# Optimization experiments

Hardware: AMD Instinct MI355X
Metric: run time of the kernel (lower is better)

The kernel has to match this reference:

```python
import jax, jax.numpy as jnp
import numpy as np

B, E, T, H = 2, 1024, 2048, 16
DH = E // H


def _conv1x1(x, W, b, mask):
    # x: [B,C,T], W: [O,C], b: [O], mask: [B,1,T] (norm=False -> plain conv on masked input)
    x = x * mask
    return jnp.einsum('oc,bct->bot', W, x) + b[None, :, None]


def setup_inputs() -> dict:
    key = jax.random.key(0)
    ks = jax.random.split(key, 16)
    inp = {
        'q': jax.random.normal(ks[0], (B, E, T), jnp.float32),
        'k': jax.random.normal(ks[1], (B, E, T), jnp.float32),
        'v': jax.random.normal(ks[2], (B, E, T), jnp.float32),
        'query_mask': (jax.random.uniform(ks[3], (B, 1, T)) < 0.9).astype(jnp.float32),
        'key_mask': (jax.random.uniform(ks[4], (B, 1, T)) < 0.9).astype(jnp.float32),
        'value_mask': (jax.random.uniform(ks[5], (B, 1, T)) < 0.9).astype(jnp.float32),
        'Wq': jax.random.normal(ks[6], (E, E), jnp.float32) * (1.0 / np.sqrt(E)),
        'bq': jnp.zeros((E,), jnp.float32),
        'Wk': jax.random.normal(ks[7], (E, E), jnp.float32) * (1.0 / np.sqrt(E)),
        'bk': jnp.zeros((E,), jnp.float32),
        'Wv': jax.random.normal(ks[8], (E, E), jnp.float32) * (1.0 / np.sqrt(E)),
        'bv': jnp.zeros((E,), jnp.float32),
        'Wo': jax.random.normal(ks[9], (E, E), jnp.float32) * (1.0 / np.sqrt(E)),
        'bo': jnp.zeros((E,), jnp.float32),
    }
    return inp


def reference(q, k, v, query_mask, key_mask, value_mask, Wq, bq, Wk, bk, Wv, bv, Wo, bo):
    # 1x1 conv projections with input masking (norm=False path)
    qp = _conv1x1(q, Wq, bq, query_mask)   # [B,E,T]
    kp = _conv1x1(k, Wk, bk, key_mask)
    vp = _conv1x1(v, Wv, bv, value_mask)
    # split heads: [B,E,T] -> [B,H,DH,T]
    qh = qp.reshape(B, H, DH, T)
    kh = kp.reshape(B, H, DH, T)
    vh = vp.reshape(B, H, DH, T)
    # scores = q^T k with pre-softmax multiplicative masks, scaled by sqrt(embed_dim)
    scores = jnp.einsum('bhdq,bhdk->bhqk', qh, kh)
    scores = scores * query_mask[:, :, :, None] * key_mask[:, :, None, :] / np.sqrt(E)
    attn = jax.nn.softmax(scores, axis=-1) * key_mask[:, :, None, :]  # post-softmax mask
    # transpose_scores=False path: v @ scores (contracts v's time dim with the query dim)
    out = jnp.einsum('bhdq,bhqk->bhdk', vh, attn)  # [B,H,DH,T]
    out = out.reshape(B, E, T)
    return _conv1x1(out, Wo, bo, key_mask)
```

## Files before the change

kernel.cpp:

```cpp
#include <hip/hip_runtime.h>

#define B 2
#define E 1024
#define T 2048
#define H 16
#define DH 64

#define SCALE2 0.0450842200277801f

typedef _Float16 f16x8 __attribute__((ext_vector_type(8)));
typedef float f32x4 __attribute__((ext_vector_type(4)));
typedef float f32x16 __attribute__((ext_vector_type(16)));
typedef unsigned short ushort8v __attribute__((ext_vector_type(8)));
typedef unsigned int uint4v __attribute__((ext_vector_type(4)));

__device__ __forceinline__ f32x4 mfma16(f16x8 a, f16x8 b, f32x4 c) {
  return __builtin_amdgcn_mfma_f32_16x16x32_f16(a, b, c, 0, 0, 0);
}
__device__ __forceinline__ f32x16 mfma32(f16x8 a, f16x8 b, f32x16 c) {
  return __builtin_amdgcn_mfma_f32_32x32x16_f16(a, b, c, 0, 0, 0);
}
__device__ __forceinline__ unsigned short f16u(float x) {
  _Float16 h = (_Float16)x;
  return __builtin_bit_cast(unsigned short, h);
}
__device__ __forceinline__ float ex2(float x) {
  return __builtin_amdgcn_exp2f(x);
}
__device__ __forceinline__ unsigned int pk16(float a, float b) {
  auto h = __builtin_amdgcn_cvt_pkrtz(a, b);
  return __builtin_bit_cast(unsigned int, h);
}

__global__ __launch_bounds__(256) void prep_weights(
    const float* __restrict__ Wq, const float* __restrict__ Wk,
    const float* __restrict__ Wv, const float* __restrict__ Wo,
    unsigned short* __restrict__ WqB, unsigned short* __restrict__ WkB,
    unsigned short* __restrict__ WvB, unsigned short* __restrict__ WoB) {
  const int which = blockIdx.y;
  const int i = (blockIdx.x * 256 + threadIdx.x) * 4;
  const float* src = which == 0 ? Wq : which == 1 ? Wk : which == 2 ? Wv : Wo;
  unsigned short* dst = which == 0 ? WqB : which == 1 ? WkB : which == 2 ? WvB : WoB;
  float4 v = *(const float4*)&src[i];
  ((unsigned int*)&dst[i])[0] = f16u(v.x) | ((unsigned)f16u(v.y) << 16);
  ((unsigned int*)&dst[i])[1] = f16u(v.z) | ((unsigned)f16u(v.w) << 16);
}

__global__ __launch_bounds__(256) void transpose_cvt(
    const float* __restrict__ q, const float* __restrict__ k,
    const float* __restrict__ v, unsigned short* __restrict__ XtQ,
    unsigned short* __restrict__ XtK, unsigned short* __restrict__ XtV) {
  __shared__ float Xs[32 * 36];
  const int z = blockIdx.z, which = z >> 1, b = z & 1;
  const float* X = which == 0 ? q : which == 1 ? k : v;
  unsigned short* O = which == 0 ? XtQ : which == 1 ? XtK : XtV;
  const int e0 = blockIdx.y * 32, t0 = blockIdx.x * 32;
  const int tid = threadIdx.x;
  const int r = tid >> 3, c = (tid & 7) * 4;
  *(float4*)&Xs[r * 36 + c] = *(const float4*)&X[((size_t)b * E + e0 + r) * T + t0 + c];
  __syncthreads();
  unsigned short h[4];
#pragma unroll
  for (int j = 0; j < 4; ++j) h[j] = f16u(Xs[(c + j) * 36 + r]);
  const size_t o = ((size_t)b * T + t0 + r) * E + e0 + c;
  ((unsigned int*)&O[o])[0] = h[0] | ((unsigned)h[1] << 16);
  ((unsigned int*)&O[o])[1] = h[2] | ((unsigned)h[3] << 16);
}

__global__ __launch_bounds__(256) void proj_qkv(
    const unsigned short* __restrict__ WqB, const unsigned short* __restrict__ WkB,
    const unsigned short* __restrict__ WvB, const unsigned short* __restrict__ XtQ,
    const unsigned short* __restrict__ XtK, const unsigned short* __restrict__ XtV,
    const float* __restrict__ bq, const float* __restrict__ bk,
    const float* __restrict__ bv, const float* __restrict__ qmask,
    const float* __restrict__ kmask, const float* __restrict__ vmask,
    unsigned short* __restrict__ qp2, unsigned short* __restrict__ kp2,
    unsigned short* __restrict__ vp) {
  __shared__ unsigned short Ah[128 * 72], Bs[128 * 72];
  const int b = blockIdx.z, my = blockIdx.y;
  const int which = my >> 3, o0 = (my & 7) * 128, t0 = blockIdx.x * 128;
  const unsigned short* W = which == 0 ? WqB : which == 1 ? WkB : WvB;
  const unsigned short* Xt = which == 0 ? XtQ : which == 1 ? XtK : XtV;
  const float* bias = which == 0 ? bq : which == 1 ? bk : bv;
  const float* mask = which == 0 ? qmask : which == 1 ? kmask : vmask;

  const int tid = threadIdx.x, wave = tid >> 6, lane = tid & 63;
  const int lg = lane & 15, quad = lane >> 4;
  const int wm = (wave & 1) * 64, wn = (wave >> 1) * 64;
  const int sr = tid >> 3, sc = (tid & 7) * 8;

  f32x4 acc[4][4];
#pragma unroll
  for (int i = 0; i < 4; ++i)
#pragma unroll
    for (int j = 0; j < 4; ++j) acc[i][j] = (f32x4){0.f, 0.f, 0.f, 0.f};

  for (int k0 = 0; k0 < E; k0 += 64) {
    ushort8v ra[4], rb[4];
#pragma unroll
    for (int p = 0; p < 4; ++p) {
      ra[p] = *(const ushort8v*)&W[(size_t)(o0 + p * 32 + sr) * E + k0 + sc];
      rb[p] = *(const ushort8v*)&Xt[((size_t)b * T + t0 + p * 32 + sr) * E + k0 + sc];
    }
    __syncthreads();
#pragma unroll
    for (int p = 0; p < 4; ++p) {
      *(ushort8v*)&Ah[(p * 32 + sr) * 72 + sc] = ra[p];
      *(ushort8v*)&Bs[(p * 32 + sr) * 72 + sc] = rb[p];
    }
    __syncthreads();
    f16x8 af[4][2];
#pragma unroll
    for (int mt = 0; mt < 4; ++mt) {
      af[mt][0] = *(const f16x8*)&Ah[(wm + mt * 16 + lg) * 72 + quad * 8];
      af[mt][1] = *(const f16x8*)&Ah[(wm + mt * 16 + lg) * 72 + 32 + quad * 8];
    }
#pragma unroll
    for (int nt = 0; nt < 4; ++nt) {
      f16x8 b0 = *(const f16x8*)&Bs[(wn + nt * 16 + lg) * 72 + quad * 8];
      f16x8 b1 = *(const f16x8*)&Bs[(wn + nt * 16 + lg) * 72 + 32 + quad * 8];
#pragma unroll
      for (int mt = 0; mt < 4; ++mt) {
        f32x4 c = acc[mt][nt];
        c = mfma16(af[mt][0], b0, c);
        c = mfma16(af[mt][1], b1, c);
        acc[mt][nt] = c;
      }
    }
  }
#pragma unroll
  for (int nt = 0; nt < 4; ++nt) {
    const int tcol = t0 + wn + nt * 16 + lg;
    const float mv = mask[b * T + tcol];
#pragma unroll
    for (int mt = 0; mt < 4; ++mt) {
      const int oF = o0 + wm + mt * 16 + quad * 4;
      float v4[4];
      if (which == 0) {
        const float s = mv * SCALE2;
#pragma unroll
        for (int r = 0; r < 4; ++r) v4[r] = (acc[mt][nt][r] + bias[oF + r]) * s;
      } else if (which == 1) {
#pragma unroll
        for (int r = 0; r < 4; ++r) v4[r] = (acc[mt][nt][r] + bias[oF + r]) * mv;
      } else {
#pragma unroll
        for (int r = 0; r < 4; ++r) v4[r] = acc[mt][nt][r] * mv + bias[oF + r];
      }
      if (which <= 1) {
        unsigned short* O = which == 0 ? qp2 : kp2;
        const int head = (o0 + wm) >> 6;
        const int bh2 = b * H + head;
        const size_t idx8 =
            (((size_t)(bh2 * (T / 32) + (tcol >> 5)) * 4 + mt) * 32 + (tcol & 31)) * 2 +
            (quad >> 1);
        unsigned int* dst = (unsigned int*)(O + idx8 * 8 + (quad & 1) * 4);
        dst[0] = f16u(v4[0]) | ((unsigned)f16u(v4[1]) << 16);
        dst[1] = f16u(v4[2]) | ((unsigned)f16u(v4[3]) << 16);
      } else {
#pragma unroll
        for (int r = 0; r < 4; ++r)
          vp[((size_t)b * E + oF + r) * T + tcol] = f16u(v4[r]);
      }
    }
  }
}

__global__ __launch_bounds__(256) void repack_v(
    const unsigned short* __restrict__ vp, unsigned short* __restrict__ vp2) {
  __shared__ unsigned short Ls[64 * 136];
  const int q0 = blockIdx.x * 128, hh = blockIdx.y, b = blockIdx.z;
  const int bh = b * H + hh;
  const int tid = threadIdx.x;
#pragma unroll
  for (int w = 0; w < 2; ++w) {
    const int d = w * 32 + (tid >> 3);
    const int c = (tid & 7) * 16;
    const unsigned short* src = vp + ((size_t)b * E + hh * DH + d) * T + q0 + c;
    *(ushort8v*)&Ls[d * 136 + c] = *(const ushort8v*)src;
    *(ushort8v*)&Ls[d * 136 + c + 8] = *(const ushort8v*)(src + 8);
  }
  __syncthreads();
#pragma unroll
  for (int w = 0; w < 4; ++w) {
    const int flat = w * 256 + tid;
    const int hb = flat & 1, lnv = (flat >> 1) & 31, dt = (flat >> 6) & 1,
              qgl = flat >> 7;
    ushort8v val = *(const ushort8v*)&Ls[(dt * 32 + lnv) * 136 + qgl * 16 + hb * 8];
    const size_t idx8 =
        (((size_t)(bh * (T / 16) + (q0 >> 4) + qgl) * 2 + dt) * 32 + lnv) * 2 + hb;
    *(ushort8v*)&vp2[idx8 * 8] = val;
  }
}

__global__ __launch_bounds__(256) void attn_stats(
    const unsigned short* __restrict__ qp2, const unsigned short* __restrict__ kp2,
    float* __restrict__ lLogOut) {
  const int bh = blockIdx.y;
  const int q0 = blockIdx.x * 128;
  const int tid = threadIdx.x, wave = tid >> 6, lane = tid & 63;
  const int ln = lane & 31, half = lane >> 5;

  const int t32q = (q0 >> 5) + wave;
  f16x8 aq[4];
#pragma unroll
  for (int s = 0; s < 4; ++s)
    aq[s] = *(const f16x8*)&qp2[((((size_t)bh * (T / 32) + t32q) * 4 + s) * 64 +
                                 ln * 2 + half) * 8];

  float lacc[16];
#pragma unroll
  for (int r = 0; r < 16; ++r) lacc[r] = 0.f;

  f16x8 bkr[2][4];
#pragma unroll
  for (int nt = 0; nt < 2; ++nt)
#pragma unroll
    for (int s = 0; s < 4; ++s)
      bkr[nt][s] = *(const f16x8*)&kp2[((((size_t)bh * (T / 32) + nt) * 4 + s) * 64 +
                                        ln * 2 + half) * 8];

  for (int kt = 0; kt < T; kt += 64) {
    const int kn = (kt + 64) & (T - 1);
    f16x8 nb[2][4];
#pragma unroll
    for (int nt = 0; nt < 2; ++nt)
#pragma unroll
      for (int s = 0; s < 4; ++s)
        nb[nt][s] =
            *(const f16x8*)&kp2[((((size_t)bh * (T / 32) + (kn >> 5) + nt) * 4 + s) * 64 +
                                 ln * 2 + half) * 8];
    f32x16 S0 = {}, S1 = {};
#pragma unroll
    for (int s = 0; s < 4; ++s) {
      S0 = mfma32(aq[s], bkr[0][s], S0);
      S1 = mfma32(aq[s], bkr[1][s], S1);
    }
#pragma unroll
    for (int r = 0; r < 16; ++r) lacc[r] += ex2(S0[r]) + ex2(S1[r]);
#pragma unroll
    for (int nt = 0; nt < 2; ++nt)
#pragma unroll
      for (int s = 0; s < 4; ++s) bkr[nt][s] = nb[nt][s];
  }
#pragma unroll
  for (int off = 1; off < 32; off <<= 1)
#pragma unroll
    for (int r = 0; r < 16; ++r) lacc[r] += __shfl_xor(lacc[r], off, 64);
  if (ln == 0) {
#pragma unroll
    for (int t = 0; t < 4; ++t) {
      f32x4 o;
#pragma unroll
      for (int j = 0; j < 4; ++j) o[j] = -__builtin_amdgcn_logf(lacc[t * 4 + j]);
      *(f32x4*)&lLogOut[(size_t)bh * T + q0 + wave * 32 + t * 8 + half * 4] = o;
    }
  }
}

__global__ __launch_bounds__(256) void attn_apply(
    const unsigned short* __restrict__ qp2, const unsigned short* __restrict__ kp2,
    const unsigned short* __restrict__ vp2, const float* __restrict__ lLog,
    unsigned short* __restrict__ ao) {
  __shared__ float st[32 * 130];
  const int bh = blockIdx.y, b = bh >> 4, h = bh & 15;
  const int kblk = blockIdx.x * 64;
  const int tid = threadIdx.x, wave = tid >> 6, lane = tid & 63;
  const int ln = lane & 31, half = lane >> 5;
  const int kt = wave & 1, qh = wave >> 1;

  const int t32k = (kblk >> 5) + kt;
  f16x8 bkk[4];
#pragma unroll
  for (int s = 0; s < 4; ++s)
    bkk[s] = *(const f16x8*)&kp2[((((size_t)bh * (T / 32) + t32k) * 4 + s) * 64 +
                                  ln * 2 + half) * 8];

  f32x16 acc0 = {}, acc1 = {};
  const int qstart = qh * (T / 2);

  f16x8 aqN[4], avN[2][2];
#pragma unroll
  for (int s = 0; s < 4; ++s)
    aqN[s] = *(const f16x8*)&qp2[((((size_t)bh * (T / 32) + (qstart >> 5)) * 4 + s) * 64 +
                                  ln * 2 + half) * 8];
#pragma unroll
  for (int dt = 0; dt < 2; ++dt)
#pragma unroll
    for (int f = 0; f < 2; ++f)
      avN[dt][f] = *(const f16x8*)&vp2[((((size_t)bh * (T / 16) + (qstart >> 4) + f) * 2 +
                                         dt) * 32 + ln) * 16 + half * 8];

  for (int qt = qstart; qt < qstart + T / 2; qt += 32) {
    f16x8 aq[4], av[2][2];
#pragma unroll
    for (int s = 0; s < 4; ++s) aq[s] = aqN[s];
#pragma unroll
    for (int dt = 0; dt < 2; ++dt)
#pragma unroll
      for (int f = 0; f < 2; ++f) av[dt][f] = avN[dt][f];
    const int qn = qt + 32 < qstart + T / 2 ? qt + 32 : qstart;
#pragma unroll
    for (int s = 0; s < 4; ++s)
      aqN[s] = *(const f16x8*)&qp2[((((size_t)bh * (T / 32) + (qn >> 5)) * 4 + s) * 64 +
                                    ln * 2 + half) * 8];
#pragma unroll
    for (int dt = 0; dt < 2; ++dt)
#pragma unroll
      for (int f = 0; f < 2; ++f)
        avN[dt][f] = *(const f16x8*)&vp2[((((size_t)bh * (T / 16) + (qn >> 4) + f) * 2 +
                                           dt) * 32 + ln) * 16 + half * 8];
    f32x4 ll[4];
#pragma unroll
    for (int t = 0; t < 4; ++t)
      ll[t] = *(const f32x4*)&lLog[(size_t)bh * T + qt + t * 8 + half * 4];
    f32x16 S = {};
#pragma unroll
    for (int s = 0; s < 4; ++s) S = mfma32(aq[s], bkk[s], S);
    unsigned int w[8];
#pragma unroll
    for (int p = 0; p < 8; ++p) {
      const float e0 = ex2(S[p * 2 + 0] + ll[p >> 1][(p & 1) * 2 + 0]);
      const float e1 = ex2(S[p * 2 + 1] + ll[p >> 1][(p & 1) * 2 + 1]);
      w[p] = pk16(e0, e1);
    }
    unsigned int x[8];
#pragma unroll
    for (int p = 0; p < 8; ++p) x[p] = __shfl_xor(w[p], 32, 64);
    uint4v f0, f1;
    f0[0] = half ? x[2] : w[0];
    f0[1] = half ? x[3] : w[1];
    f0[2] = half ? w[2] : x[0];
    f0[3] = half ? w[3] : x[1];
    f1[0] = half ? x[6] : w[4];
    f1[1] = half ? x[7] : w[5];
    f1[2] = half ? w[6] : x[4];
    f1[3] = half ? w[7] : x[5];
    const f16x8 pf0 = __builtin_bit_cast(f16x8, f0);
    const f16x8 pf1 = __builtin_bit_cast(f16x8, f1);
    acc0 = mfma32(av[0][0], pf0, acc0);
    acc0 = mfma32(av[0][1], pf1, acc0);
    acc1 = mfma32(av[1][0], pf0, acc1);
    acc1 = mfma32(av[1][1], pf1, acc1);
  }

  __syncthreads();
  if (qh == 1) {
#pragma unroll
    for (int i = 0; i < 16; ++i) {
      st[i * 130 + kt * 65 + lane] = acc0[i];
      st[(16 + i) * 130 + kt * 65 + lane] = acc1[i];
    }
  }
  __syncthreads();
  if (qh == 0) {
#pragma unroll
    for (int i = 0; i < 16; ++i) {
      acc0[i] += st[i * 130 + kt * 65 + lane];
      acc1[i] += st[(16 + i) * 130 + kt * 65 + lane];
    }
    const int kcol = kblk + kt * 32 + ln;
    const size_t obase = ((size_t)b * T + kcol) * E + h * DH;
#pragma unroll
    for (int dt = 0; dt < 2; ++dt) {
      const float* a = dt ? (const float*)&acc1 : (const float*)&acc0;
#pragma unroll
      for (int t = 0; t < 4; ++t) {
        uint2 wv;
        wv.x = f16u(a[t * 4 + 0]) | ((unsigned)f16u(a[t * 4 + 1]) << 16);
        wv.y = f16u(a[t * 4 + 2]) | ((unsigned)f16u(a[t * 4 + 3]) << 16);
        *(uint2*)&ao[obase + dt * 32 + t * 8 + half * 4] = wv;
      }
    }
  }
}

__global__ __launch_bounds__(256) void proj_final(
    const unsigned short* __restrict__ WoB, const unsigned short* __restrict__ ao,
    const float* __restrict__ bo, const float* __restrict__ kmask,
    float* __restrict__ out) {
  __shared__ unsigned short As[64 * 68], Bs[128 * 68];
  const int b = blockIdx.z, o0 = blockIdx.y * 64, t0 = blockIdx.x * 128;
  const int tid = threadIdx.x, wave = tid >> 6, lane = tid & 63;
  const int ln = lane & 31, half = lane >> 5;
  const int wn = wave * 32;
  const int ar = tid >> 2, ac = (tid & 3) * 16;
  const int br = tid >> 1, bc = (tid & 1) * 32;

  f32x16 acc0 = {}, acc1 = {};

  for (int k0 = 0; k0 < E; k0 += 64) {
    ushort8v a0 = *(const ushort8v*)&WoB[(size_t)(o0 + ar) * E + k0 + ac];
    ushort8v a1 = *(const ushort8v*)&WoB[(size_t)(o0 + ar) * E + k0 + ac + 8];
    ushort8v b0 = *(const ushort8v*)&ao[((size_t)b * T + t0 + br) * E + k0 + bc];
    ushort8v b1 = *(const ushort8v*)&ao[((size_t)b * T + t0 + br) * E + k0 + bc + 8];
    ushort8v b2 = *(const ushort8v*)&ao[((size_t)b * T + t0 + br) * E + k0 + bc + 16];
    ushort8v b3 = *(const ushort8v*)&ao[((size_t)b * T + t0 + br) * E + k0 + bc + 24];
    __syncthreads();
    *(ushort8v*)&As[ar * 68 + ac] = a0;
    *(ushort8v*)&As[ar * 68 + ac + 8] = a1;
    *(ushort8v*)&Bs[br * 68 + bc] = b0;
    *(ushort8v*)&Bs[br * 68 + bc + 8] = b1;
    *(ushort8v*)&Bs[br * 68 + bc + 16] = b2;
    *(ushort8v*)&Bs[br * 68 + bc + 24] = b3;
    __syncthreads();
#pragma unroll
    for (int s = 0; s < 4; ++s) {
      f16x8 af0 = *(const f16x8*)&As[ln * 68 + s * 16 + half * 8];
      f16x8 af1 = *(const f16x8*)&As[(32 + ln) * 68 + s * 16 + half * 8];
      f16x8 bf = *(const f16x8*)&Bs[(wn + ln) * 68 + s * 16 + half * 8];
      acc0 = mfma32(af0, bf, acc0);
      acc1 = mfma32(af1, bf, acc1);
    }
  }
  const int tcol = t0 + wn + ln;
  const float mv = kmask[b * T + tcol];
#pragma unroll
  for (int dt = 0; dt < 2; ++dt) {
    const float* a = dt ? (const float*)&acc1 : (const float*)&acc0;
#pragma unroll
    for (int t = 0; t < 4; ++t)
#pragma unroll
      for (int j = 0; j < 4; ++j) {
        const int e = o0 + dt * 32 + t * 8 + half * 4 + j;
        out[((size_t)b * E + e) * T + tcol] = a[t * 4 + j] * mv + bo[e];
      }
  }
}

extern "C" void kernel_launch(void* const* d_in, const int* in_sizes, int n_in,
                              void* d_out, int out_size, void* d_ws, size_t ws_size,
                              hipStream_t stream) {
  const float* q = (const float*)d_in[0];
  const float* k = (const float*)d_in[1];
  const float* v = (const float*)d_in[2];
  const float* qmask = (const float*)d_in[3];
  const float* kmask = (const float*)d_in[4];
  const float* vmask = (const float*)d_in[5];
  const float* Wq = (const float*)d_in[6];
  const float* bq = (const float*)d_in[7];
  const float* Wk = (const float*)d_in[8];
  const float* bk = (const float*)d_in[9];
  const float* Wv = (const float*)d_in[10];
  const float* bv = (const float*)d_in[11];
  const float* Wo = (const float*)d_in[12];
  const float* bo = (const float*)d_in[13];

  char* w = (char*)d_ws;
  const size_t WB = (size_t)E * E * sizeof(unsigned short);
  const size_t TB = (size_t)B * T * E * sizeof(unsigned short);
  unsigned short* WqB = (unsigned short*)(w + 0 * WB);
  unsigned short* WkB = (unsigned short*)(w + 1 * WB);
  unsigned short* WvB = (unsigned short*)(w + 2 * WB);
  unsigned short* WoB = (unsigned short*)(w + 3 * WB);
  size_t off = 4 * WB;
  unsigned short* XtQ = (unsigned short*)(w + off); off += TB;
  unsigned short* XtK = (unsigned short*)(w + off); off += TB;
  unsigned short* XtV = (unsigned short*)(w + off); off += TB;
  unsigned short* qp2 = (unsigned short*)(w + off); off += TB;
  unsigned short* kp2 = (unsigned short*)(w + off); off += TB;
  unsigned short* vp  = (unsigned short*)(w + off); off += TB;
  unsigned short* vp2 = (unsigned short*)(w + off); off += TB;
  float* lLog = (float*)(w + off); off += (size_t)B * H * T * sizeof(float);
  unsigned short* ao = XtQ;

  dim3 bl(256);
  prep_weights<<<dim3((E * E) / 1024, 4), bl, 0, stream>>>(
      Wq, Wk, Wv, Wo, WqB, WkB, WvB, WoB);
  transpose_cvt<<<dim3(T / 32, E / 32, 3 * B), bl, 0, stream>>>(
      q, k, v, XtQ, XtK, XtV);
  proj_qkv<<<dim3(T / 128, 24, B), bl, 0, stream>>>(
      WqB, WkB, WvB, XtQ, XtK, XtV, bq, bk, bv, qmask, kmask, vmask, qp2, kp2, vp);
  repack_v<<<dim3(T / 128, H, B), bl, 0, stream>>>(vp, vp2);
  attn_stats<<<dim3(T / 128, B * H), bl, 0, stream>>>(qp2, kp2, lLog);
  attn_apply<<<dim3(T / 64, B * H), bl, 0, stream>>>(qp2, kp2, vp2, lLog, ao);
  proj_final<<<dim3(T / 128, E / 64, B), bl, 0, stream>>>(
      WoB, ao, bo, kmask, (float*)d_out);
}
```

Measured before the change: 284.3 us.

## Split attention stats and apply kernels across two reduction halves with merge kernels

Both attention kernels gain a z grid dimension that splits the reduction range (key range for stats, query range for apply) in two. Partial results go to fp32 scratch and are combined by two new merge kernels. This doubles the grid (512 to 1024 blocks for stats, 1024 to 2048 for apply) to fill more CUs and shortens each block's serial loop. It also swaps the shfl_xor half-exchange for permlane32_swap, prefetches the lLog row one iteration ahead, and sets a min-blocks launch bound. The cost is two extra launches and extra fp32 partial traffic, with the workspace reshuffled so aPart reuses the XtK/XtV space.

```diff
diff --git a/kernel.cpp b/kernel.cpp
--- a/kernel.cpp
+++ b/kernel.cpp
@@ -30,6 +30,11 @@
 __device__ __forceinline__ unsigned int pk16(float a, float b) {
   auto h = __builtin_amdgcn_cvt_pkrtz(a, b);
   return __builtin_bit_cast(unsigned int, h);
+}
+__device__ __forceinline__ void plswap(unsigned int& a, unsigned int& b) {
+  auto r = __builtin_amdgcn_permlane32_swap(a, b, false, false);
+  a = r[0];
+  b = r[1];
 }
 
 __global__ __launch_bounds__(256) void prep_weights(
@@ -195,8 +200,9 @@
 
 __global__ __launch_bounds__(256) void attn_stats(
     const unsigned short* __restrict__ qp2, const unsigned short* __restrict__ kp2,
-    float* __restrict__ lLogOut) {
+    float* __restrict__ sPart) {
   const int bh = blockIdx.y;
+  const int z = blockIdx.z;
   const int q0 = blockIdx.x * 128;
   const int tid = threadIdx.x, wave = tid >> 6, lane = tid & 63;
   const int ln = lane & 31, half = lane >> 5;
@@ -212,16 +218,19 @@
 #pragma unroll
   for (int r = 0; r < 16; ++r) lacc[r] = 0.f;
 
+  const int kbase = z * (T / 2);
+  const int kend = kbase + T / 2;
+
   f16x8 bkr[2][4];
 #pragma unroll
   for (int nt = 0; nt < 2; ++nt)
 #pragma unroll
     for (int s = 0; s < 4; ++s)
-      bkr[nt][s] = *(const f16x8*)&kp2[((((size_t)bh * (T / 32) + nt) * 4 + s) * 64 +
-                                        ln * 2 + half) * 8];
-
-  for (int kt = 0; kt < T; kt += 64) {
-    const int kn = (kt + 64) & (T - 1);
+      bkr[nt][s] = *(const f16x8*)&kp2[((((size_t)bh * (T / 32) + (kbase >> 5) + nt) * 4 +
+                                         s) * 64 + ln * 2 + half) * 8];
+
+  for (int kt = kbase; kt < kend; kt += 64) {
+    const int kn = (kt + 64 < kend) ? kt + 64 : kbase;
     f16x8 nb[2][4];
 #pragma unroll
     for (int nt = 0; nt < 2; ++nt)
@@ -252,18 +261,32 @@
     for (int t = 0; t < 4; ++t) {
       f32x4 o;
 #pragma unroll
-      for (int j = 0; j < 4; ++j) o[j] = -__builtin_amdgcn_logf(lacc[t * 4 + j]);
-      *(f32x4*)&lLogOut[(size_t)bh * T + q0 + wave * 32 + t * 8 + half * 4] = o;
-    }
-  }
-}
-
-__global__ __launch_bounds__(256) void attn_apply(
+      for (int j = 0; j < 4; ++j) o[j] = lacc[t * 4 + j];
+      *(f32x4*)&sPart[((size_t)z * (B * H) + bh) * T + q0 + wave * 32 + t * 8 +
+                      half * 4] = o;
+    }
+  }
+}
+
+__global__ __launch_bounds__(256) void stats_merge(
+    const float* __restrict__ sPart, float* __restrict__ lLog) {
+  const int i = (blockIdx.x * 256 + threadIdx.x) * 4;
+  const int N = B * H * T;
+  f32x4 a = *(const f32x4*)&sPart[i];
+  f32x4 b = *(const f32x4*)&sPart[N + i];
+  f32x4 o;
+#pragma unroll
+  for (int j = 0; j < 4; ++j) o[j] = -__builtin_amdgcn_logf(a[j] + b[j]);
+  *(f32x4*)&lLog[i] = o;
+}
+
+__global__ __launch_bounds__(256, 5) void attn_apply(
     const unsigned short* __restrict__ qp2, const unsigned short* __restrict__ kp2,
     const unsigned short* __restrict__ vp2, const float* __restrict__ lLog,
-    unsigned short* __restrict__ ao) {
+    float* __restrict__ aPart) {
   __shared__ float st[32 * 130];
-  const int bh = blockIdx.y, b = bh >> 4, h = bh & 15;
+  const int bh = blockIdx.y;
+  const int z = blockIdx.z;
   const int kblk = blockIdx.x * 64;
   const int tid = threadIdx.x, wave = tid >> 6, lane = tid & 63;
   const int ln = lane & 31, half = lane >> 5;
@@ -277,9 +300,11 @@
                                   ln * 2 + half) * 8];
 
   f32x16 acc0 = {}, acc1 = {};
-  const int qstart = qh * (T / 2);
+  const int qstart = (z * 2 + qh) * (T / 4);
+  const int qend = qstart + T / 4;
 
   f16x8 aqN[4], avN[2][2];
+  f32x4 llN[4];
 #pragma unroll
   for (int s = 0; s < 4; ++s)
     aqN[s] = *(const f16x8*)&qp2[((((size_t)bh * (T / 32) + (qstart >> 5)) * 4 + s) * 64 +
@@ -290,16 +315,22 @@
     for (int f = 0; f < 2; ++f)
       avN[dt][f] = *(const f16x8*)&vp2[((((size_t)bh * (T / 16) + (qstart >> 4) + f) * 2 +
                                          dt) * 32 + ln) * 16 + half * 8];
-
-  for (int qt = qstart; qt < qstart + T / 2; qt += 32) {
+#pragma unroll
+  for (int t = 0; t < 4; ++t)
+    llN[t] = *(const f32x4*)&lLog[(size_t)bh * T + qstart + t * 8 + half * 4];
+
+  for (int qt = qstart; qt < qend; qt += 32) {
     f16x8 aq[4], av[2][2];
+    f32x4 ll[4];
 #pragma unroll
     for (int s = 0; s < 4; ++s) aq[s] = aqN[s];
 #pragma unroll
     for (int dt = 0; dt < 2; ++dt)
 #pragma unroll
       for (int f = 0; f < 2; ++f) av[dt][f] = avN[dt][f];
-    const int qn = qt + 32 < qstart + T / 2 ? qt + 32 : qstart;
+#pragma unroll
+    for (int t = 0; t < 4; ++t) ll[t] = llN[t];
+    const int qn = qt + 32 < qend ? qt + 32 : qstart;
 #pragma unroll
     for (int s = 0; s < 4; ++s)
       aqN[s] = *(const f16x8*)&qp2[((((size_t)bh * (T / 32) + (qn >> 5)) * 4 + s) * 64 +
@@ -310,10 +341,9 @@
       for (int f = 0; f < 2; ++f)
         avN[dt][f] = *(const f16x8*)&vp2[((((size_t)bh * (T / 16) + (qn >> 4) + f) * 2 +
                                            dt) * 32 + ln) * 16 + half * 8];
-    f32x4 ll[4];
 #pragma unroll
     for (int t = 0; t < 4; ++t)
-      ll[t] = *(const f32x4*)&lLog[(size_t)bh * T + qt + t * 8 + half * 4];
+      llN[t] = *(const f32x4*)&lLog[(size_t)bh * T + qn + t * 8 + half * 4];
     f32x16 S = {};
 #pragma unroll
     for (int s = 0; s < 4; ++s) S = mfma32(aq[s], bkk[s], S);
@@ -324,18 +354,13 @@
       const float e1 = ex2(S[p * 2 + 1] + ll[p >> 1][(p & 1) * 2 + 1]);
       w[p] = pk16(e0, e1);
     }
-    unsigned int x[8];
-#pragma unroll
-    for (int p = 0; p < 8; ++p) x[p] = __shfl_xor(w[p], 32, 64);
+    plswap(w[0], w[2]);
+    plswap(w[1], w[3]);
+    plswap(w[4], w[6]);
+    plswap(w[5], w[7]);
     uint4v f0, f1;
-    f0[0] = half ? x[2] : w[0];
-    f0[1] = half ? x[3] : w[1];
-    f0[2] = half ? w[2] : x[0];
-    f0[3] = half ? w[3] : x[1];
-    f1[0] = half ? x[6] : w[4];
-    f1[1] = half ? x[7] : w[5];
-    f1[2] = half ? w[6] : x[4];
-    f1[3] = half ? w[7] : x[5];
+    f0[0] = w[0]; f0[1] = w[1]; f0[2] = w[2]; f0[3] = w[3];
+    f1[0] = w[4]; f1[1] = w[5]; f1[2] = w[6]; f1[3] = w[7];
     const f16x8 pf0 = __builtin_bit_cast(f16x8, f0);
     const f16x8 pf1 = __builtin_bit_cast(f16x8, f1);
     acc0 = mfma32(av[0][0], pf0, acc0);
@@ -360,19 +385,43 @@
       acc1[i] += st[(16 + i) * 130 + kt * 65 + lane];
     }
     const int kcol = kblk + kt * 32 + ln;
-    const size_t obase = ((size_t)b * T + kcol) * E + h * DH;
+    float* dst = aPart + ((size_t)(z * B * H + bh) * T + kcol) * DH;
 #pragma unroll
     for (int dt = 0; dt < 2; ++dt) {
       const float* a = dt ? (const float*)&acc1 : (const float*)&acc0;
 #pragma unroll
       for (int t = 0; t < 4; ++t) {
-        uint2 wv;
-        wv.x = f16u(a[t * 4 + 0]) | ((unsigned)f16u(a[t * 4 + 1]) << 16);
-        wv.y = f16u(a[t * 4 + 2]) | ((unsigned)f16u(a[t * 4 + 3]) << 16);
-        *(uint2*)&ao[obase + dt * 32 + t * 8 + half * 4] = wv;
+        f32x4 o;
+#pragma unroll
+        for (int j = 0; j < 4; ++j) o[j] = a[t * 4 + j];
+        *(f32x4*)&dst[dt * 32 + t * 8 + half * 4] = o;
       }
     }
   }
+}
+
+__global__ __launch_bounds__(256) void apply_merge(
+    const float* __restrict__ aPart, unsigned short* __restrict__ ao) {
+  const size_t i = ((size_t)blockIdx.x * 256 + threadIdx.x) * 8;
+  const size_t NZ = (size_t)B * H * T * DH;
+  f32x4 a0 = *(const f32x4*)&aPart[i];
+  f32x4 a1 = *(const f32x4*)&aPart[i + 4];
+  f32x4 b0 = *(const f32x4*)&aPart[NZ + i];
+  f32x4 b1 = *(const f32x4*)&aPart[NZ + i + 4];
+  unsigned short h[8];
+#pragma unroll
+  for (int j = 0; j < 4; ++j) h[j] = f16u(a0[j] + b0[j]);
+#pragma unroll
+  for (int j = 0; j < 4; ++j) h[4 + j] = f16u(a1[j] + b1[j]);
+  const int bh = (int)(i >> 17);
+  const int rem = (int)(i & (T * DH - 1));
+  const int k = rem >> 6, d = rem & 63;
+  uint4v u;
+  u[0] = h[0] | ((unsigned)h[1] << 16);
+  u[1] = h[2] | ((unsigned)h[3] << 16);
+  u[2] = h[4] | ((unsigned)h[5] << 16);
+  u[3] = h[6] | ((unsigned)h[7] << 16);
+  *(uint4v*)&ao[((size_t)(bh >> 4) * T + k) * E + (bh & 15) * 64 + d] = u;
 }
 
 __global__ __launch_bounds__(256) void proj_final(
@@ -455,13 +504,15 @@
   unsigned short* WoB = (unsigned short*)(w + 3 * WB);
   size_t off = 4 * WB;
   unsigned short* XtQ = (unsigned short*)(w + off); off += TB;
+  unsigned short* qp2 = (unsigned short*)(w + off); off += TB;
+  unsigned short* kp2 = (unsigned short*)(w + off); off += TB;
+  unsigned short* vp2 = (unsigned short*)(w + off); off += TB;
+  float* lLog = (float*)(w + off); off += (size_t)B * H * T * sizeof(float);
+  float* sPart = (float*)(w + off); off += (size_t)2 * B * H * T * sizeof(float);
   unsigned short* XtK = (unsigned short*)(w + off); off += TB;
   unsigned short* XtV = (unsigned short*)(w + off); off += TB;
-  unsigned short* qp2 = (unsigned short*)(w + off); off += TB;
-  unsigned short* kp2 = (unsigned short*)(w + off); off += TB;
   unsigned short* vp  = (unsigned short*)(w + off); off += TB;
-  unsigned short* vp2 = (unsigned short*)(w + off); off += TB;
-  float* lLog = (float*)(w + off); off += (size_t)B * H * T * sizeof(float);
+  float* aPart = (float*)XtK;
   unsigned short* ao = XtQ;
 
   dim3 bl(256);
@@ -472,8 +523,10 @@
   proj_qkv<<<dim3(T / 128, 24, B), bl, 0, stream>>>(
       WqB, WkB, WvB, XtQ, XtK, XtV, bq, bk, bv, qmask, kmask, vmask, qp2, kp2, vp);
   repack_v<<<dim3(T / 128, H, B), bl, 0, stream>>>(vp, vp2);
-  attn_stats<<<dim3(T / 128, B * H), bl, 0, stream>>>(qp2, kp2, lLog);
-  attn_apply<<<dim3(T / 64, B * H), bl, 0, stream>>>(qp2, kp2, vp2, lLog, ao);
+  attn_stats<<<dim3(T / 128, B * H, 2), bl, 0, stream>>>(qp2, kp2, sPart);
+  stats_merge<<<dim3((B * H * T) / 1024), bl, 0, stream>>>(sPart, lLog);
+  attn_apply<<<dim3(T / 64, B * H, 2), bl, 0, stream>>>(qp2, kp2, vp2, lLog, aPart);
+  apply_merge<<<dim3((B * H * T * DH) / 2048), bl, 0, stream>>>(aPart, ao);
   proj_final<<<dim3(T / 128, E / 64, B), bl, 0, stream>>>(
       WoB, ao, bo, kmask, (float*)d_out);
 }
```

Result: slower. 326.9 us (+15.0%).
